# Performance work log

Measured on AMD Instinct MI355X. Metric: run time of the kernel, lower is better.

Reference implementation:

```python
import jax, jax.numpy as jnp
import numpy as np

NT = 16          # nt_states
TS = 48          # t_states
T = NT + TS      # total states
B, N = 4, 24     # batch, sentence length
HUGE = 1.0e9


def setup_inputs():
    key = jax.random.key(0)
    k1, k2, k3 = jax.random.split(key, 3)
    unary_scores = jax.nn.log_softmax(jax.random.normal(k1, (B, N, T), jnp.float32), axis=-1)
    rule = jax.random.normal(k2, (B, NT, N, T, T, 2), jnp.float32)
    rule_scores = jax.nn.log_softmax(rule.reshape(B, NT, N, -1), axis=-1).reshape(B, NT, N, T, T, 2)
    root_scores = jax.nn.log_softmax(jax.random.normal(k3, (B, NT), jnp.float32), axis=-1)
    return {"unary_scores": unary_scores, "rule_scores": rule_scores, "root_scores": root_scores}


def _lse(x, axes):
    return jax.nn.logsumexp(x, axis=axes)


def _inside(unary_scores, rule_scores, root_scores):
    Bv, Nv, Tt = unary_scores.shape
    nt = rule_scores.shape[1]
    dt = unary_scores.dtype
    R = jnp.moveaxis(rule_scores, 5, 0)            # (D, B, Tparent, H, TL, TR)

    # beta[b,l,r,t,h]: headed inside chart; betau[b,l,r,t]: head-summed chart
    beta = jnp.full((Bv, Nv + 1, Nv + 1, Tt, Nv), -HUGE, dt)
    betau = jnp.full((Bv, Nv + 1, Nv + 1, Tt), -HUGE, dt)

    # width-1 spans: only terminal states (word_span_slice = nt:T, nt_emission=False)
    ks = np.arange(Nv)
    st = np.arange(nt, Tt)
    beta = beta.at[:, ks[:, None], ks[:, None] + 1, st[None, :], ks[:, None]].set(0.0)
    betau = betau.at[:, ks[:, None], ks[:, None] + 1, st[None, :]].set(
        unary_scores[:, ks[:, None], st[None, :]])

    nts = np.arange(nt)
    for W in range(2, Nv + 1):
        L = Nv - W + 1
        ls = np.arange(L)
        rs = ls + W
        hidx = ls[:, None] + np.arange(W)          # (L, W) absolute head positions

        def width_body(beta, betau, R, unary_scores, W=W, ls=ls, rs=rs, hidx=hidx):
            def chartH(la, ra, s0, s1):            # (B, L, S, W)
                x = beta[:, la, ra, s0:s1, :]
                return jnp.take_along_axis(x, hidx[None, :, None, :], axis=3)

            def chartU(la, ra, s0, s1):            # (B, L, S)
                return betau[:, la, ra, s0:s1]

            def rwin(d, a0, a1, c0, c1):           # (B, L, nt, W, A, C)
                r = R[d][:, :, hidx, a0:a1, c0:c1]
                return jnp.transpose(r, (0, 2, 1, 3, 4, 5))

            def comb(xH, yU, xU, yH, z0, z1):
                # D=0: head from left child; D=1: head from right child.
                # logsumexp over TL, TR and both directions -> (B, L, nt, W)
                left = (jnp.transpose(xH, (0, 1, 3, 2))[:, :, None, :, :, None]
                        + yU[:, :, None, None, None, :] + z0)
                right = (xU[:, :, None, None, :, None]
                         + jnp.transpose(yH, (0, 1, 3, 2))[:, :, None, :, None, :] + z1)
                return jnp.logaddexp(_lse(left, (-2, -1)), _lse(right, (-2, -1)))

            c0, c1 = (nt, Tt) if W == 2 else (0, nt)
            # split at l+1: left child is a single terminal
            tmp = comb(chartH(ls, ls + 1, nt, Tt), chartU(ls + 1, rs, c0, c1),
                       chartU(ls, ls + 1, nt, Tt), chartH(ls + 1, rs, c0, c1),
                       rwin(0, nt, Tt, c0, c1), rwin(1, nt, Tt, c0, c1))
            if W >= 3:
                # split at r-1: right child is a single terminal
                tmp = jnp.logaddexp(tmp, comb(
                    chartH(ls, rs - 1, 0, nt), chartU(rs - 1, rs, nt, Tt),
                    chartU(ls, rs - 1, 0, nt), chartH(rs - 1, rs, nt, Tt),
                    rwin(0, 0, nt, nt, Tt), rwin(1, 0, nt, nt, Tt)))
            if W >= 4:
                # interior splits: both children are nonterminal spans
                z0 = rwin(0, 0, nt, 0, nt)
                z1 = rwin(1, 0, nt, 0, nt)
                for wl in range(2, W - 1):
                    s = ls + wl
                    tmp = jnp.logaddexp(tmp, comb(
                        chartH(ls, s, 0, nt), chartU(s, rs, 0, nt),
                        chartU(ls, s, 0, nt), chartH(s, rs, 0, nt), z0, z1))
            # add head-word emission under the parent NT; sum heads for betau
            uw = jnp.transpose(unary_scores[:, hidx, :nt], (0, 1, 3, 2))  # (B,L,nt,W)
            return tmp, _lse(tmp + uw, -1)

        tmp, tmpu = jax.checkpoint(width_body)(beta, betau, R, unary_scores)
        beta = beta.at[:, ls[:, None, None], rs[:, None, None],
                       nts[None, :, None], hidx[:, None, :]].set(tmp)
        betau = betau.at[:, ls[:, None], rs[:, None], nts[None, :]].set(tmpu)

    return jax.nn.logsumexp(betau[:, 0, Nv, :nt] + root_scores, axis=-1)  # log Z, (B,)


_inside_jit = jax.jit(_inside)


def reference(unary_scores, rule_scores, root_scores):
    return _inside_jit(unary_scores, rule_scores, root_scores)
```

## Files before the change

kernel.cpp:

```cpp
#include <hip/hip_runtime.h>
#include <cstddef>

#define Bv 4
#define Nv 24
#define NTv 16
#define Tv 64
#define NP 25
#define NEGF (-1e30f)

#define BETAA_OFF 0
#define BETAU_OFF 960000
#define RNT_OFF   1120000
#define T0_OFF    1906432
#define T1_OFF    2496256
#define T0L_OFF   3086080
#define T1R_OFF   3110656
#define D0_OFF    3135232
#define D1_OFF    3136768
#define EU_OFF    3138304
#define CELLF_OFF 3142912
#define WS_NEED   3145412

__device__ __forceinline__ void publish(float* p, float v) {
  __hip_atomic_store(p, v, __ATOMIC_RELAXED, __HIP_MEMORY_SCOPE_AGENT);
}

__device__ __forceinline__ unsigned packbf2(float lo, float hi) {
  unsigned bl = __float_as_uint(lo), bh = __float_as_uint(hi);
  bl = (bl + 0x7FFFu + ((bl >> 16) & 1u)) >> 16;
  bh = (bh + 0x7FFFu + ((bh >> 16) & 1u)) >> 16;
  return (bh << 16) | bl;
}

__global__ void init_kernel(const float* __restrict__ unary, float* __restrict__ betau,
                            float* __restrict__ Eu, int* __restrict__ cellF) {
  int t = blockIdx.x * blockDim.x + threadIdx.x;
  if (t < Bv * NP * NP) cellF[t] = 0;
  if (t >= Bv * Nv * 48) return;
  int i = t % 48, kk = (t / 48) % Nv, b = t / (48 * Nv);
  float u = unary[(size_t)(b * Nv + kk) * Tv + 16 + i];
  betau[((size_t)(b * NP + kk) * NP + (kk + 1)) * Tv + 16 + i] = u;
  Eu[(size_t)(b * Nv + kk) * 48 + i] = __expf(u);
}

__global__ __launch_bounds__(256) void prep_kernel(
    const float* __restrict__ rule, const float* __restrict__ Eu,
    unsigned* __restrict__ RNTh, float* __restrict__ T0, float* __restrict__ T1,
    float* __restrict__ T0L, float* __restrict__ T1R,
    float* __restrict__ D0, float* __restrict__ D1) {
  const int h = blockIdx.x, A = blockIdx.y, b = blockIdx.z;
  const int t = threadIdx.x;
  __shared__ float er0[64 * 65];
  __shared__ float er1[64 * 65];
  __shared__ float E[24 * 48];
  __shared__ float red[256];

  for (int i = t; i < 24 * 48; i += 256) E[i] = Eu[(size_t)b * (24 * 48) + i];
  const float* rb = rule + (size_t)((b * NTv + A) * Nv + h) * 8192;
#pragma unroll
  for (int i = 0; i < 8; ++i) {
    int lin = i * 1024 + t * 4;
    float4 v = *(const float4*)(rb + lin);
    int sL = lin >> 7, rem = (lin & 127) >> 1;
    er0[sL * 65 + rem] = __expf(v.x);
    er1[sL * 65 + rem] = __expf(v.y);
    er0[sL * 65 + rem + 1] = __expf(v.z);
    er1[sL * 65 + rem + 1] = __expf(v.w);
  }
  __syncthreads();
  {
    unsigned* dst0 = RNTh + (((size_t)(b * 2 + 0) * Nv + h) * NTv + A) * 128;
    unsigned* dst1 = RNTh + (((size_t)(b * 2 + 1) * Nv + h) * NTv + A) * 128;
    if (t < 128) {
      int sL = t >> 3, sRp = t & 7;
      dst0[t] = packbf2(er0[sL * 65 + 2 * sRp], er0[sL * 65 + 2 * sRp + 1]);
    } else {
      int t2 = t - 128;
      int sL = t2 >> 3, sRp = t2 & 7;
      dst1[t2] = packbf2(er1[sL * 65 + 2 * sRp], er1[sL * 65 + 2 * sRp + 1]);
    }
  }
  for (int o = t; o < 384; o += 256) {
    int p = o >> 4, sL = o & 15;
    const float* Ep = E + p * 48;
    const float* r0 = er0 + sL * 65 + 16;
    float acc = 0.f;
#pragma unroll 8
    for (int j = 0; j < 48; ++j) acc += Ep[j] * r0[j];
    T0[(((size_t)(b * Nv + h) * Nv + p) * NTv + sL) * NTv + A] = acc;
  }
  for (int o = t; o < 384; o += 256) {
    int p = o >> 4, sR = o & 15;
    const float* Ep = E + p * 48;
    float acc = 0.f;
#pragma unroll 8
    for (int i = 0; i < 48; ++i) acc += Ep[i] * er1[(16 + i) * 65 + sR];
    T1[(((size_t)(b * Nv + h) * Nv + p) * NTv + sR) * NTv + A] = acc;
  }
  if (t < 16) {
    float acc = 0.f;
    for (int i = 0; i < 48; ++i) acc += er0[(16 + i) * 65 + t];
    T0L[((size_t)(b * Nv + h) * NTv + t) * NTv + A] = acc;
  } else if (t < 32) {
    int sL = t - 16;
    float acc = 0.f;
    for (int j = 0; j < 48; ++j) acc += er1[sL * 65 + 16 + j];
    T1R[((size_t)(b * Nv + h) * NTv + sL) * NTv + A] = acc;
  }
  float acc0 = 0.f, acc1 = 0.f;
  const int hp = (h + 1 < 24) ? h + 1 : 0, hm = (h >= 1) ? h - 1 : 0;
  for (int e = t; e < 2304; e += 256) {
    int i = e / 48, j = e % 48;
    float r0 = er0[(16 + i) * 65 + 16 + j];
    float r1 = er1[(16 + i) * 65 + 16 + j];
    acc0 += E[hp * 48 + j] * r0;
    acc1 += E[hm * 48 + i] * r1;
  }
  red[t] = acc0;
  __syncthreads();
  if (t < 64) {
    float s = red[t] + red[t + 64] + red[t + 128] + red[t + 192];
#pragma unroll
    for (int off = 32; off; off >>= 1) s += __shfl_xor(s, off, 64);
    if (t == 0 && h <= 22) D0[((size_t)b * Nv + h) * NTv + A] = s;
  }
  __syncthreads();
  red[t] = acc1;
  __syncthreads();
  if (t < 64) {
    float s = red[t] + red[t + 64] + red[t + 128] + red[t + 192];
#pragma unroll
    for (int off = 32; off; off >>= 1) s += __shfl_xor(s, off, 64);
    if (t == 0 && h >= 1) D1[((size_t)b * Nv + (h - 1)) * NTv + A] = s;
  }
}

__device__ __forceinline__ float max16(float v) {
  v = fmaxf(v, __shfl_xor(v, 8, 16));
  v = fmaxf(v, __shfl_xor(v, 4, 16));
  v = fmaxf(v, __shfl_xor(v, 2, 16));
  v = fmaxf(v, __shfl_xor(v, 1, 16));
  return v;
}

__device__ __forceinline__ void edge_dot(float v0, float v1, float v2, float v3,
                                         const float* Tb, float& sh, float& S) {
  float mx = fmaxf(fmaxf(v0, v1), fmaxf(v2, v3));
  mx = fmaxf(mx, __shfl_xor(mx, 1, 64));
  mx = fmaxf(mx, __shfl_xor(mx, 2, 64));
  float dot = __expf(v0 - mx) * Tb[0] + __expf(v1 - mx) * Tb[16] +
              __expf(v2 - mx) * Tb[32] + __expf(v3 - mx) * Tb[48];
  dot += __shfl_xor(dot, 1, 64);
  dot += __shfl_xor(dot, 2, 64);
  sh = mx;
  S = dot;
}

#define MAXI 21

__global__ __launch_bounds__(768) void width_all_kernel(
    const float* __restrict__ unary, float* __restrict__ betaA, float* __restrict__ betau,
    const unsigned* __restrict__ RNTh, const float* __restrict__ T0, const float* __restrict__ T1,
    const float* __restrict__ T0L, const float* __restrict__ T1R,
    const float* __restrict__ D0, const float* __restrict__ D1,
    const float* __restrict__ root, float* __restrict__ out, int* __restrict__ cellF) {
  const int rr = blockIdx.x, b = blockIdx.y;
  const int r = rr + 2;
  const int tid = threadIdx.x;
  int* flagb = cellF + b * (NP * NP);

  __shared__ float chartC[23][384];
  __shared__ float buC[23][16];
  __shared__ float U0[24 * 256], U1[24 * 256];
  __shared__ float sG0[24], sG1[24];
  __shared__ float pM[2 * 24 * 16], pS[2 * 24 * 16];
  __shared__ float sTmp[16 * 24];

  for (int i = 0; i <= r - 2; ++i) {
    const int l = r - 2 - i;
    const int W = r - l;

    if (W >= 4) {
      if (tid < W - 3) {
        const int m = l + 2 + tid;
        while (__hip_atomic_load(&flagb[l * NP + m], __ATOMIC_RELAXED,
                                 __HIP_MEMORY_SCOPE_AGENT) == 0)
          __builtin_amdgcn_s_sleep(1);
      }
      __syncthreads();
    }

    const int g = tid >> 5;
    const int k = tid & 31;
    float U0r[8], U1r[8];
#pragma unroll
    for (int j = 0; j < 8; ++j) { U0r[j] = 0.f; U1r[j] = 0.f; }
    float G0 = NEGF, G1 = NEGF;

    if (g < W) {
      const int hcol = l + g;
      float av1[MAXI], av0[MAXI];
      int e1 = min(l + g, r - 2);
      int cnt1 = e1 - (l + 2) + 1; if (cnt1 < 0) cnt1 = 0;
      if (k < 16) {
        const size_t base = ((size_t)(b * NP + l) * NP + (l + 2)) * Tv + k;
#pragma unroll
        for (int ii = 0; ii < MAXI; ++ii)
          if (ii < cnt1) av1[ii] = betau[base + (size_t)ii * Tv];
      } else {
#pragma unroll
        for (int ii = 0; ii < MAXI; ++ii)
          if (ii < cnt1) av1[ii] = chartC[l + 2 + ii][hcol * 16 + (k - 16)];
      }
      int m0 = max(l + g + 1, l + 2), e0 = r - 2;
      int cnt0 = e0 - m0 + 1; if (cnt0 < 0) cnt0 = 0;
      if (k < 16) {
        const size_t base = ((size_t)(b * NP + l) * NP + m0) * 384 + (size_t)hcol * 16 + k;
#pragma unroll
        for (int ii = 0; ii < MAXI; ++ii)
          if (ii < cnt0) av0[ii] = betaA[base + (size_t)ii * 384];
      } else {
#pragma unroll
        for (int ii = 0; ii < MAXI; ++ii)
          if (ii < cnt0) av0[ii] = buC[m0 + ii][k - 16];
      }
      float mx1 = NEGF, mx0 = NEGF;
#pragma unroll
      for (int ii = 0; ii < MAXI; ++ii) {
        if (ii < cnt1) mx1 = fmaxf(mx1, av1[ii]);
        if (ii < cnt0) mx0 = fmaxf(mx0, av0[ii]);
      }
      float o1 = max16(mx1), o0 = max16(mx0);
      float t1 = __shfl_xor(o1, 16, 32), t0 = __shfl_xor(o0, 16, 32);
      G1 = o1 + t1;
      G0 = o0 + t0;
#pragma unroll
      for (int ii = 0; ii < MAXI; ++ii) {
        if (ii < cnt1) {
          float e = __expf(av1[ii] - o1);
          float eR = __shfl(e, 16 + (k & 15), 32);
#pragma unroll
          for (int j = 0; j < 8; ++j)
            U1r[j] += __shfl(e, 2 * j + (k >> 4), 32) * eR;
        }
        if (ii < cnt0) {
          float e = __expf(av0[ii] - o0);
          float eR = __shfl(e, 16 + (k & 15), 32);
#pragma unroll
          for (int j = 0; j < 8; ++j)
            U0r[j] += __shfl(e, 2 * j + (k >> 4), 32) * eR;
        }
      }
#pragma unroll
      for (int j = 0; j < 8; ++j) {
        U0[g * 256 + k + 32 * j] = U0r[j];
        U1[g * 256 + k + 32 * j] = U1r[j];
      }
      if (k == 0) { sG0[g] = G0; sG1[g] = G1; }
    }
    __syncthreads();

    {
      if (W >= 3) {
        while (__hip_atomic_load(&flagb[l * NP + (r - 1)], __ATOMIC_RELAXED,
                                 __HIP_MEMORY_SCOPE_AGENT) == 0)
          __builtin_amdgcn_s_sleep(1);
      }
      const int w = tid >> 6, lane = tid & 63;
      const int A = lane >> 2, q = lane & 3;
      for (int p = w; p < 2 * W; p += 12) {
        const int hh = p >> 1, d = p & 1;
        const int h = l + hh;
        const float* Urow = (d ? U1 : U0) + hh * 256 + 4 * q;
        const unsigned* Rb = RNTh + (((size_t)(b * 2 + d) * Nv + h) * NTv + A) * 128 + 2 * q;
        float a0 = 0.f, a1 = 0.f, a2 = 0.f, a3 = 0.f;
#pragma unroll
        for (int sL = 0; sL < 16; ++sL) {
          float4 u = *(const float4*)(Urow + sL * 16);
          uint2 rv = *(const uint2*)(Rb + sL * 8);
          float r0 = __uint_as_float(rv.x << 16);
          float r1 = __uint_as_float(rv.x & 0xFFFF0000u);
          float r2 = __uint_as_float(rv.y << 16);
          float r3 = __uint_as_float(rv.y & 0xFFFF0000u);
          a0 += u.x * r0; a1 += u.y * r1; a2 += u.z * r2; a3 += u.w * r3;
        }
        float acc = (a0 + a1) + (a2 + a3);
        acc += __shfl_xor(acc, 1, 64);
        acc += __shfl_xor(acc, 2, 64);
        float Mi = d ? sG1[hh] : sG0[hh];
        float sh2 = NEGF, S2 = 0.f, sh3 = NEGF, S3 = 0.f;
        if (W >= 3) {
          if (d == 0) {
            if (hh < W - 1) {
              const float* Tb = T0 + (((size_t)(b * Nv + h) * Nv + (r - 1)) * NTv + 4 * q) * NTv + A;
              float4 e4 = *(const float4*)(betaA +
                  ((size_t)(b * NP + l) * NP + (r - 1)) * 384 + (size_t)h * 16 + 4 * q);
              edge_dot(e4.x, e4.y, e4.z, e4.w, Tb, sh2, S2);
            }
            if (hh == 0) {
              const float* Tb = T0L + ((size_t)(b * Nv + l) * NTv + 4 * q) * NTv + A;
              const float* u4 = &buC[l + 1][4 * q];
              edge_dot(u4[0], u4[1], u4[2], u4[3], Tb, sh3, S3);
            }
          } else {
            if (hh >= 1) {
              const float* Tb = T1 + (((size_t)(b * Nv + h) * Nv + l) * NTv + 4 * q) * NTv + A;
              const float* e4 = &chartC[l + 1][h * 16 + 4 * q];
              edge_dot(e4[0], e4[1], e4[2], e4[3], Tb, sh2, S2);
            }
            if (hh == W - 1) {
              const float* Tb = T1R + ((size_t)(b * Nv + (r - 1)) * NTv + 4 * q) * NTv + A;
              float4 u4 = *(const float4*)(betau +
                  ((size_t)(b * NP + l) * NP + (r - 1)) * Tv + 4 * q);
              edge_dot(u4.x, u4.y, u4.z, u4.w, Tb, sh3, S3);
            }
          }
        } else {
          if (d == 0 && hh == 0) { sh2 = 0.f; S2 = D0[((size_t)b * Nv + l) * NTv + A]; }
          if (d == 1 && hh == 1) { sh2 = 0.f; S2 = D1[((size_t)b * Nv + l) * NTv + A]; }
        }
        float Mf = fmaxf(Mi, fmaxf(sh2, sh3));
        float Sf = acc * __expf(Mi - Mf) + S2 * __expf(sh2 - Mf) + S3 * __expf(sh3 - Mf);
        if (q == 0) {
          pM[(d * 24 + hh) * 16 + A] = Mf;
          pS[(d * 24 + hh) * 16 + A] = Sf;
        }
      }
    }
    __syncthreads();

    if (tid < 384) {
      int A2 = tid & 15, hh = tid >> 4;
      if (hh < W) {
        float M0 = pM[(0 * 24 + hh) * 16 + A2], S0 = pS[(0 * 24 + hh) * 16 + A2];
        float M1 = pM[(1 * 24 + hh) * 16 + A2], S1 = pS[(1 * 24 + hh) * 16 + A2];
        float nm = fmaxf(M0, M1);
        float s = S0 * __expf(M0 - nm) + S1 * __expf(M1 - nm);
        float val = nm + __logf(s);
        publish(&betaA[((size_t)(b * NP + l) * NP + r) * 384 + (l + hh) * 16 + A2], val);
        chartC[l][(l + hh) * 16 + A2] = val;
        sTmp[A2 * 24 + hh] = val + unary[(size_t)(b * Nv + (l + hh)) * Tv + A2];
      }
    }
    __syncthreads();
    if (tid < 16) {
      float mx = NEGF;
      for (int x = 0; x < W; ++x) mx = fmaxf(mx, sTmp[tid * 24 + x]);
      float s = 0.f;
      for (int x = 0; x < W; ++x) s += __expf(sTmp[tid * 24 + x] - mx);
      float val = mx + __logf(s);
      publish(&betau[((size_t)(b * NP + l) * NP + r) * Tv + tid], val);
      buC[l][tid] = val;
    }
    if (tid == 0) {
      asm volatile("s_waitcnt vmcnt(0)" ::: "memory");
      __hip_atomic_store(&flagb[l * NP + r], 1, __ATOMIC_RELAXED,
                         __HIP_MEMORY_SCOPE_AGENT);
    }
  }

  if (rr == 22) {
    __syncthreads();
    if (tid == 0) {
      float vals[NTv];
      float mx = NEGF;
#pragma unroll
      for (int A = 0; A < NTv; ++A) {
        float v = buC[0][A] + root[b * NTv + A];
        vals[A] = v;
        mx = fmaxf(mx, v);
      }
      float s = 0.f;
#pragma unroll
      for (int A = 0; A < NTv; ++A) s += __expf(vals[A] - mx);
      out[b] = mx + __logf(s);
    }
  }
}

__global__ __launch_bounds__(768) void width_kernel_fb(
    const float* __restrict__ unary, const float* __restrict__ rule,
    float* __restrict__ betaA, float* __restrict__ betau, int W) {
  const int l = blockIdx.x, b = blockIdx.y;
  const int r = l + W;
  const int tid = threadIdx.x;
  const int sub = tid & 1;
  const int pid = tid >> 1;
  const int A = pid & 15;
  const int hh = pid >> 4;
  const int h = l + hh;
  const bool act = (hh < W);
  const int sA = tid & 15, sH = tid >> 4;

  __shared__ float sER0[48], sEL1[48];
  __shared__ float sCL0[16 * 24], sCR1[16 * 24];
  __shared__ float sMaxL0[24], sMaxR1[24];
  __shared__ float sShR0, sShL1;
  __shared__ float sTmp[16 * 24];

  float runM = NEGF, runS = 0.f;
  for (int m = l + 1; m < r; ++m) {
    const int wl = m - l, wr = r - m;
    if (tid < 64) {
      const int n = (wr == 1) ? 48 : 16, s0 = (wr == 1) ? 16 : 0;
      float v = (tid < n) ? betau[(size_t)((b * NP + m) * NP + r) * Tv + s0 + tid] : NEGF;
      float mx = v;
#pragma unroll
      for (int off = 32; off; off >>= 1) mx = fmaxf(mx, __shfl_xor(mx, off, 64));
      if (tid == 0) sShR0 = mx;
      if (tid < n) sER0[tid] = v - mx;
    } else if (tid < 128) {
      const int j = tid - 64;
      const int n = (wl == 1) ? 48 : 16, s0 = (wl == 1) ? 16 : 0;
      float v = (j < n) ? betau[(size_t)((b * NP + l) * NP + m) * Tv + s0 + j] : NEGF;
      float mx = v;
#pragma unroll
      for (int off = 32; off; off >>= 1) mx = fmaxf(mx, __shfl_xor(mx, off, 64));
      if (j == 0) sShL1 = mx;
      if (j < n) sEL1[j] = v - mx;
    }
    if (tid < 384) {
      if (wl > 1 && sH < wl) {
        float v = betaA[(size_t)((b * NP + l) * NP + m) * 384 + sA * Nv + (l + sH)];
        float mx = v;
#pragma unroll
        for (int off = 8; off; off >>= 1) mx = fmaxf(mx, __shfl_xor(mx, off, 16));
        if (sA == 0) sMaxL0[sH] = mx;
        sCL0[sA * Nv + sH] = v - mx;
      }
      if (wr > 1 && sH >= wl && sH < W) {
        float v = betaA[(size_t)((b * NP + m) * NP + r) * 384 + sA * Nv + (l + sH)];
        float mx = v;
#pragma unroll
        for (int off = 8; off; off >>= 1) mx = fmaxf(mx, __shfl_xor(mx, off, 16));
        if (sA == 0) sMaxR1[sH] = mx;
        sCR1[sA * Nv + sH] = v - mx;
      }
    }
    __syncthreads();
    if (act) {
      if (hh < wl && (wl > 1 || hh == 0)) {
        const int nL = (wl == 1) ? 48 : 16, sL0 = (wl == 1) ? 16 : 0;
        const int nR = (wr == 1) ? 48 : 16, sR0 = (wr == 1) ? 16 : 0;
        const float shift = ((wl == 1) ? 0.f : sMaxL0[hh]) + sShR0;
        float part = 0.f;
        const float* rb = rule + (size_t)(((b * NTv + A) * Nv + h) * Tv) * Tv * 2;
        for (int i = sub; i < nL; i += 2) {
          const float cl = (wl == 1) ? 0.f : sCL0[i * Nv + hh];
          const float* rp = rb + (size_t)(sL0 + i) * Tv * 2 + sR0 * 2;
#pragma unroll 8
          for (int j = 0; j < nR; ++j) part += __expf(cl + sER0[j] + rp[j * 2]);
        }
        float nm = fmaxf(runM, shift);
        runS = runS * __expf(runM - nm) + part * __expf(shift - nm);
        runM = nm;
      }
      if (hh >= wl && (wr > 1 || hh == W - 1)) {
        const int nL = (wl == 1) ? 48 : 16, sL0 = (wl == 1) ? 16 : 0;
        const int nR = (wr == 1) ? 48 : 16, sR0 = (wr == 1) ? 16 : 0;
        const float shift = sShL1 + ((wr == 1) ? 0.f : sMaxR1[hh]);
        float part = 0.f;
        const float* rb = rule + (size_t)(((b * NTv + A) * Nv + h) * Tv) * Tv * 2 + 1;
        for (int i = sub; i < nL; i += 2) {
          const float el = sEL1[i];
          const float* rp = rb + (size_t)(sL0 + i) * Tv * 2 + sR0 * 2;
#pragma unroll 8
          for (int j = 0; j < nR; ++j) {
            const float cr = (wr == 1) ? 0.f : sCR1[j * Nv + hh];
            part += __expf(el + cr + rp[j * 2]);
          }
        }
        float nm = fmaxf(runM, shift);
        runS = runS * __expf(runM - nm) + part * __expf(shift - nm);
        runM = nm;
      }
    }
    __syncthreads();
  }
  if (act) {
    float om = __shfl_xor(runM, 1, 64);
    float os = __shfl_xor(runS, 1, 64);
    float nm = fmaxf(runM, om);
    float s = runS * __expf(runM - nm) + os * __expf(om - nm);
    if (sub == 0) {
      float val = nm + __logf(s);
      betaA[(size_t)((b * NP + l) * NP + r) * 384 + A * Nv + h] = val;
      sTmp[A * Nv + hh] = val + unary[(b * Nv + h) * Tv + A];
    }
  }
  __syncthreads();
  if (tid < 16) {
    float mx = NEGF;
    for (int x = 0; x < W; ++x) mx = fmaxf(mx, sTmp[tid * Nv + x]);
    float s = 0.f;
    for (int x = 0; x < W; ++x) s += __expf(sTmp[tid * Nv + x] - mx);
    betau[(size_t)((b * NP + l) * NP + r) * Tv + tid] = mx + __logf(s);
  }
}

__global__ void final_kernel(const float* __restrict__ betau, const float* __restrict__ root,
                             float* __restrict__ out) {
  int b = threadIdx.x;
  if (b < Bv) {
    float vals[NTv];
    float mx = NEGF;
#pragma unroll
    for (int A = 0; A < NTv; ++A) {
      float v = betau[(size_t)((b * NP + 0) * NP + Nv) * Tv + A] + root[b * NTv + A];
      vals[A] = v;
      mx = fmaxf(mx, v);
    }
    float s = 0.f;
#pragma unroll
    for (int A = 0; A < NTv; ++A) s += __expf(vals[A] - mx);
    out[b] = mx + __logf(s);
  }
}

extern "C" void kernel_launch(void* const* d_in, const int* in_sizes, int n_in,
                              void* d_out, int out_size, void* d_ws, size_t ws_size,
                              hipStream_t stream) {
  (void)in_sizes; (void)n_in; (void)out_size;
  const float* unary = (const float*)d_in[0];
  const float* rule  = (const float*)d_in[1];
  const float* root  = (const float*)d_in[2];
  float* out = (float*)d_out;
  float* ws = (float*)d_ws;
  float* betaA = ws + BETAA_OFF;
  float* betau = ws + BETAU_OFF;
  const bool fast = ws_size >= (size_t)WS_NEED * sizeof(float);

  if (fast) {
    unsigned* RNTh = (unsigned*)(ws + RNT_OFF);
    float* T0  = ws + T0_OFF;
    float* T1  = ws + T1_OFF;
    float* T0L = ws + T0L_OFF;
    float* T1R = ws + T1R_OFF;
    float* D0  = ws + D0_OFF;
    float* D1  = ws + D1_OFF;
    float* Eu  = ws + EU_OFF;
    int* cellF = (int*)(ws + CELLF_OFF);
    init_kernel<<<(Bv * Nv * 48 + 255) / 256, 256, 0, stream>>>(unary, betau, Eu, cellF);
    prep_kernel<<<dim3(24, 16, 4), 256, 0, stream>>>(rule, Eu, RNTh, T0, T1, T0L, T1R, D0, D1);
    void* args[] = {(void*)&unary, (void*)&betaA, (void*)&betau, (void*)&RNTh,
                    (void*)&T0, (void*)&T1, (void*)&T0L, (void*)&T1R,
                    (void*)&D0, (void*)&D1, (void*)&root, (void*)&out, (void*)&cellF};
    hipLaunchCooperativeKernel((const void*)width_all_kernel, dim3(Nv - 1, Bv), dim3(768),
                               args, 0, stream);
  } else {
    float* Eu = ws + BETAU_OFF + 160000;
    int* prog = (int*)(ws + BETAU_OFF + 160000 + 4608);
    init_kernel<<<(Bv * Nv * 48 + 255) / 256, 256, 0, stream>>>(unary, betau, Eu, prog);
    for (int W = 2; W <= Nv; ++W) {
      dim3 grid(Nv - W + 1, Bv);
      width_kernel_fb<<<grid, 768, 0, stream>>>(unary, rule, betaA, betau, W);
    }
    final_kernel<<<1, 64, 0, stream>>>(betau, root, out);
  }
}
```

Measured before the change: 464.6 us.

## Compute split outer products and rule contraction with bf16 MFMA per wave

Replaces the shuffle-based outer-product accumulation over split points with one 16x16x32 bf16 MFMA per (head, direction) pair, with each wave owning its pairs so the shared-memory G arrays and one block barrier go away. The rule contraction against the packed bf16 rule table is also moved onto MFMA. There the U operand is only filled in the sym==0 column, so the instruction effectively computes a matrix-vector product, and results are redistributed with shuffles. Exponentiated split scores are now rounded to bf16 before accumulation, which loses precision. The max is taken per whole span rather than per state, which risks underflow, and split counts above 32 would be silently dropped.

Measured after the change: 406.7 us. 12.5% less time.

```diff
diff --git a/kernel.cpp b/kernel.cpp
--- a/kernel.cpp
+++ b/kernel.cpp
@@ -7,6 +7,10 @@
 #define Tv 64
 #define NP 25
 #define NEGF (-1e30f)
+
+typedef __attribute__((ext_vector_type(8))) short short8v;
+typedef __attribute__((ext_vector_type(4))) float f32x4;
+union FragU { unsigned u[4]; short8v s; };
 
 #define BETAA_OFF 0
 #define BETAU_OFF 960000
@@ -135,14 +139,6 @@
   }
 }
 
-__device__ __forceinline__ float max16(float v) {
-  v = fmaxf(v, __shfl_xor(v, 8, 16));
-  v = fmaxf(v, __shfl_xor(v, 4, 16));
-  v = fmaxf(v, __shfl_xor(v, 2, 16));
-  v = fmaxf(v, __shfl_xor(v, 1, 16));
-  return v;
-}
-
 __device__ __forceinline__ void edge_dot(float v0, float v1, float v2, float v3,
                                          const float* Tb, float& sh, float& S) {
   float mx = fmaxf(fmaxf(v0, v1), fmaxf(v2, v3));
@@ -156,8 +152,6 @@
   S = dot;
 }
 
-#define MAXI 21
-
 __global__ __launch_bounds__(768) void width_all_kernel(
     const float* __restrict__ unary, float* __restrict__ betaA, float* __restrict__ betau,
     const unsigned* __restrict__ RNTh, const float* __restrict__ T0, const float* __restrict__ T1,
@@ -172,15 +166,18 @@
   __shared__ float chartC[23][384];
   __shared__ float buC[23][16];
   __shared__ float U0[24 * 256], U1[24 * 256];
-  __shared__ float sG0[24], sG1[24];
   __shared__ float pM[2 * 24 * 16], pS[2 * 24 * 16];
   __shared__ float sTmp[16 * 24];
+
+  const int wv = tid >> 6, lane = tid & 63;
+  const int sym = lane & 15;
+  const int mBlk = (lane >> 4) * 8;
 
   for (int i = 0; i <= r - 2; ++i) {
     const int l = r - 2 - i;
     const int W = r - l;
 
-    if (W >= 4) {
+    if (W >= 3) {
       if (tid < W - 3) {
         const int m = l + 2 + tid;
         while (__hip_atomic_load(&flagb[l * NP + m], __ATOMIC_RELAXED,
@@ -190,104 +187,107 @@
       __syncthreads();
     }
 
-    const int g = tid >> 5;
-    const int k = tid & 31;
-    float U0r[8], U1r[8];
-#pragma unroll
-    for (int j = 0; j < 8; ++j) { U0r[j] = 0.f; U1r[j] = 0.f; }
-    float G0 = NEGF, G1 = NEGF;
-
-    if (g < W) {
-      const int hcol = l + g;
-      float av1[MAXI], av0[MAXI];
-      int e1 = min(l + g, r - 2);
-      int cnt1 = e1 - (l + 2) + 1; if (cnt1 < 0) cnt1 = 0;
-      if (k < 16) {
-        const size_t base = ((size_t)(b * NP + l) * NP + (l + 2)) * Tv + k;
-#pragma unroll
-        for (int ii = 0; ii < MAXI; ++ii)
-          if (ii < cnt1) av1[ii] = betau[base + (size_t)ii * Tv];
-      } else {
-#pragma unroll
-        for (int ii = 0; ii < MAXI; ++ii)
-          if (ii < cnt1) av1[ii] = chartC[l + 2 + ii][hcol * 16 + (k - 16)];
-      }
-      int m0 = max(l + g + 1, l + 2), e0 = r - 2;
-      int cnt0 = e0 - m0 + 1; if (cnt0 < 0) cnt0 = 0;
-      if (k < 16) {
-        const size_t base = ((size_t)(b * NP + l) * NP + m0) * 384 + (size_t)hcol * 16 + k;
-#pragma unroll
-        for (int ii = 0; ii < MAXI; ++ii)
-          if (ii < cnt0) av0[ii] = betaA[base + (size_t)ii * 384];
-      } else {
-#pragma unroll
-        for (int ii = 0; ii < MAXI; ++ii)
-          if (ii < cnt0) av0[ii] = buC[m0 + ii][k - 16];
-      }
-      float mx1 = NEGF, mx0 = NEGF;
-#pragma unroll
-      for (int ii = 0; ii < MAXI; ++ii) {
-        if (ii < cnt1) mx1 = fmaxf(mx1, av1[ii]);
-        if (ii < cnt0) mx0 = fmaxf(mx0, av0[ii]);
-      }
-      float o1 = max16(mx1), o0 = max16(mx0);
-      float t1 = __shfl_xor(o1, 16, 32), t0 = __shfl_xor(o0, 16, 32);
-      G1 = o1 + t1;
-      G0 = o0 + t0;
-#pragma unroll
-      for (int ii = 0; ii < MAXI; ++ii) {
-        if (ii < cnt1) {
-          float e = __expf(av1[ii] - o1);
-          float eR = __shfl(e, 16 + (k & 15), 32);
-#pragma unroll
-          for (int j = 0; j < 8; ++j)
-            U1r[j] += __shfl(e, 2 * j + (k >> 4), 32) * eR;
+    float Gp[4];
+#pragma unroll
+    for (int pi = 0; pi < 4; ++pi) {
+      const int p = wv + 12 * pi;
+      if (p < 2 * W) {
+        const int hh = p >> 1, d = p & 1, hcol = l + hh;
+        int mst, cnt;
+        if (d) { mst = l + 2; cnt = min(l + hh, r - 2) - mst + 1; }
+        else   { mst = max(l + hh + 1, l + 2); cnt = (r - 2) - mst + 1; }
+        if (cnt < 0) cnt = 0;
+        float* Ua = (d ? U1 : U0) + hh * 256;
+        if (cnt == 0) {
+#pragma unroll
+          for (int reg = 0; reg < 4; ++reg)
+            Ua[((lane >> 4) * 4 + reg) * 16 + sym] = 0.f;
+          Gp[pi] = -2e30f;
+        } else {
+          float Lv[8], Rv[8];
+          if (d) {
+            const size_t lb = ((size_t)(b * NP + l) * NP + mst) * Tv + sym;
+#pragma unroll
+            for (int j = 0; j < 8; ++j) {
+              int mi = mBlk + j;
+              Lv[j] = (mi < cnt) ? betau[lb + (size_t)mi * Tv] : NEGF;
+              Rv[j] = (mi < cnt) ? chartC[mst + mi][hcol * 16 + sym] : NEGF;
+            }
+          } else {
+            const size_t lb = ((size_t)(b * NP + l) * NP + mst) * 384 + hcol * 16 + sym;
+#pragma unroll
+            for (int j = 0; j < 8; ++j) {
+              int mi = mBlk + j;
+              Lv[j] = (mi < cnt) ? betaA[lb + (size_t)mi * 384] : NEGF;
+              Rv[j] = (mi < cnt) ? buC[mst + mi][sym] : NEGF;
+            }
+          }
+          float mxL = NEGF, mxR = NEGF;
+#pragma unroll
+          for (int j = 0; j < 8; ++j) { mxL = fmaxf(mxL, Lv[j]); mxR = fmaxf(mxR, Rv[j]); }
+#pragma unroll
+          for (int off = 1; off < 64; off <<= 1) {
+            mxL = fmaxf(mxL, __shfl_xor(mxL, off, 64));
+            mxR = fmaxf(mxR, __shfl_xor(mxR, off, 64));
+          }
+          FragU fa, fb;
+#pragma unroll
+          for (int jj = 0; jj < 4; ++jj) {
+            int m0i = mBlk + 2 * jj, m1i = m0i + 1;
+            float e0 = (m0i < cnt) ? __expf(Lv[2 * jj] - mxL) : 0.f;
+            float e1 = (m1i < cnt) ? __expf(Lv[2 * jj + 1] - mxL) : 0.f;
+            fa.u[jj] = packbf2(e0, e1);
+            float f0 = (m0i < cnt) ? __expf(Rv[2 * jj] - mxR) : 0.f;
+            float f1 = (m1i < cnt) ? __expf(Rv[2 * jj + 1] - mxR) : 0.f;
+            fb.u[jj] = packbf2(f0, f1);
+          }
+          f32x4 z = {0.f, 0.f, 0.f, 0.f};
+          f32x4 dU = __builtin_amdgcn_mfma_f32_16x16x32_bf16(fa.s, fb.s, z, 0, 0, 0);
+#pragma unroll
+          for (int reg = 0; reg < 4; ++reg)
+            Ua[((lane >> 4) * 4 + reg) * 16 + sym] = dU[reg];
+          Gp[pi] = mxL + mxR;
         }
-        if (ii < cnt0) {
-          float e = __expf(av0[ii] - o0);
-          float eR = __shfl(e, 16 + (k & 15), 32);
-#pragma unroll
-          for (int j = 0; j < 8; ++j)
-            U0r[j] += __shfl(e, 2 * j + (k >> 4), 32) * eR;
+      }
+    }
+
+    if (W >= 3) {
+      while (__hip_atomic_load(&flagb[l * NP + (r - 1)], __ATOMIC_RELAXED,
+                               __HIP_MEMORY_SCOPE_AGENT) == 0)
+        __builtin_amdgcn_s_sleep(1);
+    }
+
+#pragma unroll
+    for (int pi = 0; pi < 4; ++pi) {
+      const int p = wv + 12 * pi;
+      if (p < 2 * W) {
+        const int hh = p >> 1, d = p & 1, h = l + hh;
+        const float* Ua = (d ? U1 : U0) + hh * 256;
+        const unsigned* Rb = RNTh + (((size_t)(b * 2 + d) * Nv + h) * NTv + sym) * 128;
+        f32x4 acc4 = {0.f, 0.f, 0.f, 0.f};
+#pragma unroll
+        for (int kk = 0; kk < 8; ++kk) {
+          uint4 ar = *(const uint4*)(Rb + kk * 16 + (lane >> 4) * 4);
+          FragU fa, fb;
+          fa.u[0] = ar.x; fa.u[1] = ar.y; fa.u[2] = ar.z; fa.u[3] = ar.w;
+          if (sym == 0) {
+            const float* up = Ua + kk * 32 + mBlk;
+#pragma unroll
+            for (int jj = 0; jj < 4; ++jj) fb.u[jj] = packbf2(up[2 * jj], up[2 * jj + 1]);
+          } else {
+            fb.u[0] = 0; fb.u[1] = 0; fb.u[2] = 0; fb.u[3] = 0;
+          }
+          acc4 = __builtin_amdgcn_mfma_f32_16x16x32_bf16(fa.s, fb.s, acc4, 0, 0, 0);
         }
-      }
-#pragma unroll
-      for (int j = 0; j < 8; ++j) {
-        U0[g * 256 + k + 32 * j] = U0r[j];
-        U1[g * 256 + k + 32 * j] = U1r[j];
-      }
-      if (k == 0) { sG0[g] = G0; sG1[g] = G1; }
-    }
-    __syncthreads();
-
-    {
-      if (W >= 3) {
-        while (__hip_atomic_load(&flagb[l * NP + (r - 1)], __ATOMIC_RELAXED,
-                                 __HIP_MEMORY_SCOPE_AGENT) == 0)
-          __builtin_amdgcn_s_sleep(1);
-      }
-      const int w = tid >> 6, lane = tid & 63;
-      const int A = lane >> 2, q = lane & 3;
-      for (int p = w; p < 2 * W; p += 12) {
-        const int hh = p >> 1, d = p & 1;
-        const int h = l + hh;
-        const float* Urow = (d ? U1 : U0) + hh * 256 + 4 * q;
-        const unsigned* Rb = RNTh + (((size_t)(b * 2 + d) * Nv + h) * NTv + A) * 128 + 2 * q;
-        float a0 = 0.f, a1 = 0.f, a2 = 0.f, a3 = 0.f;
-#pragma unroll
-        for (int sL = 0; sL < 16; ++sL) {
-          float4 u = *(const float4*)(Urow + sL * 16);
-          uint2 rv = *(const uint2*)(Rb + sL * 8);
-          float r0 = __uint_as_float(rv.x << 16);
-          float r1 = __uint_as_float(rv.x & 0xFFFF0000u);
-          float r2 = __uint_as_float(rv.y << 16);
-          float r3 = __uint_as_float(rv.y & 0xFFFF0000u);
-          a0 += u.x * r0; a1 += u.y * r1; a2 += u.z * r2; a3 += u.w * r3;
-        }
-        float acc = (a0 + a1) + (a2 + a3);
-        acc += __shfl_xor(acc, 1, 64);
-        acc += __shfl_xor(acc, 2, 64);
-        float Mi = d ? sG1[hh] : sG0[hh];
+        const int A = lane >> 2, q = lane & 3;
+        const int src = (A >> 2) << 4;
+        float c0 = __shfl(acc4[0], src, 64);
+        float c1 = __shfl(acc4[1], src, 64);
+        float c2 = __shfl(acc4[2], src, 64);
+        float c3 = __shfl(acc4[3], src, 64);
+        const int sel = A & 3;
+        float acc = (sel == 0) ? c0 : (sel == 1) ? c1 : (sel == 2) ? c2 : c3;
+        float Mi = Gp[pi];
         float sh2 = NEGF, S2 = 0.f, sh3 = NEGF, S3 = 0.f;
         if (W >= 3) {
           if (d == 0) {
```
